# Kernel optimization log

Measured on AMD Instinct MI355X. Metric: run time of the kernel, lower is better.

## Reference

```python
import jax, jax.numpy as jnp
import numpy as np

EMBED = 768
HEADS = 12
HEAD_DIM = EMBED // HEADS
SCALE = HEAD_DIM ** -0.5


def setup_inputs() -> dict:
    key = jax.random.key(0)
    k1, k2, k3, k4, k5 = jax.random.split(key, 5)
    x = jax.random.normal(k1, (4, 2048, EMBED), dtype=jnp.float32)
    w_qkv = jax.random.normal(k2, (EMBED, 3 * EMBED), dtype=jnp.float32) * (EMBED ** -0.5)
    b_qkv = jax.random.normal(k3, (3 * EMBED,), dtype=jnp.float32) * 0.02
    w_proj = jax.random.normal(k4, (EMBED, EMBED), dtype=jnp.float32) * (EMBED ** -0.5)
    b_proj = jax.random.normal(k5, (EMBED,), dtype=jnp.float32) * 0.02
    return {"x": x, "w_qkv": w_qkv, "b_qkv": b_qkv, "w_proj": w_proj, "b_proj": b_proj}


def reference(x, w_qkv, b_qkv, w_proj, b_proj):
    B, T, D = x.shape
    qkv = x @ w_qkv + b_qkv                      # [B, T, 3D]
    qkv = qkv.reshape(B, T, 3, HEADS, HEAD_DIM)
    qkv = jnp.transpose(qkv, (2, 0, 3, 1, 4))    # [3, B, H, T, hd]
    q, k, v = qkv[0], qkv[1], qkv[2]
    scores = jnp.einsum('bhqd,bhkd->bhqk', q, k) * SCALE
    attn = jax.nn.softmax(scores, axis=-1)       # dropout p=0.0 -> identity
    out = jnp.einsum('bhqk,bhkd->bhqd', attn, v)
    out = jnp.transpose(out, (0, 2, 1, 3)).reshape(B, T, D)
    return out @ w_proj + b_proj
```

## Files before the change

### kernel.cpp

```cpp
#include <hip/hip_runtime.h>
#include <hip/hip_bf16.h>

#define EMBED 768
#define HEADS 12
#define HD 64
#define BATCH 4
#define SEQ 2048
#define M_TOK (BATCH*SEQ)
#define N_QKV (3*EMBED)
#define SL2E 0.18033688011112042f

typedef short bf8 __attribute__((ext_vector_type(8)));
typedef float f4  __attribute__((ext_vector_type(4)));
typedef unsigned short us8 __attribute__((ext_vector_type(8)));

static __device__ inline unsigned short f2bf(float f) {
    unsigned int x = __float_as_uint(f);
    unsigned int r = (x + 0x7fffu + ((x >> 16) & 1u)) >> 16;
    return (unsigned short)r;
}

static __device__ inline unsigned int pack2bf(float a, float b) {
#if defined(__has_builtin)
#if __has_builtin(__builtin_amdgcn_cvt_pk_bf16_f32)
    auto r = __builtin_amdgcn_cvt_pk_bf16_f32(a, b);
    return __builtin_bit_cast(unsigned int, r);
#else
    unsigned int ua = (__float_as_uint(a) + 0x8000u) >> 16;
    unsigned int ub = (__float_as_uint(b) + 0x8000u) & 0xffff0000u;
    return ua | ub;
#endif
#else
    unsigned int ua = (__float_as_uint(a) + 0x8000u) >> 16;
    unsigned int ub = (__float_as_uint(b) + 0x8000u) & 0xffff0000u;
    return ua | ub;
#endif
}

#define GLD_LDS(gp, lp) __builtin_amdgcn_global_load_lds( \
    (const __attribute__((address_space(1))) void*)(gp),  \
    (__attribute__((address_space(3))) void*)(lp), 16, 0, 0)

__global__ void cvt_f32_bf16(const float* __restrict__ in,
                             unsigned short* __restrict__ out, int n) {
    int i = (blockIdx.x * blockDim.x + threadIdx.x) * 4;
    if (i < n) {
        float4 v = *reinterpret_cast<const float4*>(in + i);
        ushort4 o;
        o.x = f2bf(v.x); o.y = f2bf(v.y); o.z = f2bf(v.z); o.w = f2bf(v.w);
        *reinterpret_cast<ushort4*>(out + i) = o;
    }
}

__global__ void transpose_f32_bf16(const float* __restrict__ in,
                                   unsigned short* __restrict__ out, int R, int C,
                                   float scale, int nlim) {
    __shared__ float tile[32][33];
    int c0 = blockIdx.x * 32, r0 = blockIdx.y * 32;
    int tx = threadIdx.x, ty = threadIdx.y;
    for (int i = 0; i < 32; i += 8)
        tile[ty + i][tx] = in[(size_t)(r0 + ty + i) * C + c0 + tx];
    __syncthreads();
    for (int i = 0; i < 32; i += 8) {
        int orow = c0 + ty + i;
        float s = (orow < nlim) ? scale : 1.0f;
        out[(size_t)orow * R + r0 + tx] = f2bf(tile[tx][ty + i] * s);
    }
}

__global__ void scale_bias(const float* __restrict__ in, float* __restrict__ out) {
    int i = blockIdx.x * 256 + threadIdx.x;
    if (i < N_QKV) out[i] = in[i] * (i < 768 ? SL2E : 1.0f);
}

template<int OUT_MODE>
__global__ __launch_bounds__(256) void gemm_bf16(
    const unsigned short* __restrict__ A,
    const unsigned short* __restrict__ BT,
    const float* __restrict__ bias,
    void* __restrict__ Cout, int M, int N, int K)
{
    const int LDA = 32;
    __shared__ unsigned short a_lds[128 * 32];
    __shared__ unsigned short b_lds[128 * 32];
    int tid  = threadIdx.x;
    int lane = tid & 63, w = tid >> 6;
    int quad = lane >> 4, cc = lane & 15;
    int m0 = blockIdx.x * 128, n0 = blockIdx.y * 128;
    int wr = w >> 1, wc = w & 1;
    int mb = wr * 64, nb = wc * 64;
    const unsigned short* Ab = A + (size_t)m0 * K;
    const unsigned short* Bb = BT + (size_t)n0 * K;
    f4 acc[4][4] = {};
    for (int k0 = 0; k0 < K; k0 += 32) {
        __syncthreads();
        for (int p = 0; p < 2; ++p) {
            int li  = p * 256 + tid;
            int row = li >> 2, ch = li & 3;
            GLD_LDS(Ab + (size_t)row * K + k0 + ch * 8, &a_lds[li * 8]);
            GLD_LDS(Bb + (size_t)row * K + k0 + ch * 8, &b_lds[li * 8]);
        }
        __syncthreads();
        bf8 af[4], bfv[4];
        for (int mi = 0; mi < 4; ++mi)
            af[mi] = *reinterpret_cast<const bf8*>(&a_lds[(mb + mi * 16 + cc) * LDA + quad * 8]);
        for (int ni = 0; ni < 4; ++ni)
            bfv[ni] = *reinterpret_cast<const bf8*>(&b_lds[(nb + ni * 16 + cc) * LDA + quad * 8]);
        for (int mi = 0; mi < 4; ++mi)
            for (int ni = 0; ni < 4; ++ni)
                acc[mi][ni] = __builtin_amdgcn_mfma_f32_16x16x32_bf16(af[mi], bfv[ni], acc[mi][ni], 0, 0, 0);
    }
    for (int mi = 0; mi < 4; ++mi)
        for (int ni = 0; ni < 4; ++ni) {
            int gn = n0 + nb + ni * 16 + cc;
            float bv = bias[gn];
            for (int r = 0; r < 4; ++r) {
                int gm = m0 + mb + mi * 16 + quad * 4 + r;
                float v = acc[mi][ni][r] + bv;
                if (OUT_MODE == 0)
                    ((unsigned short*)Cout)[(size_t)gm * N + gn] = f2bf(v);
                else
                    ((float*)Cout)[(size_t)gm * N + gn] = v;
            }
        }
}

__global__ __launch_bounds__(256) void vtrans(
    const unsigned short* __restrict__ qkv, unsigned short* __restrict__ vt)
{
    __shared__ unsigned short lds[64 * 72];
    int tid = threadIdx.x;
    int t0 = blockIdx.x * 64, h = blockIdx.y, b = blockIdx.z;
    for (int p = 0; p < 2; ++p) {
        int li = p * 256 + tid, row = li >> 3, col = li & 7;
        *reinterpret_cast<uint4*>(&lds[row * 72 + col * 8]) =
            *reinterpret_cast<const uint4*>(
                qkv + (size_t)(b * SEQ + t0 + row) * 2304 + 1536 + h * 64 + col * 8);
    }
    __syncthreads();
    for (int p = 0; p < 2; ++p) {
        int li = p * 256 + tid, d = li >> 3, tc = li & 7;
        us8 v;
        for (int j = 0; j < 8; ++j) v[j] = lds[(tc * 8 + j) * 72 + d];
        *reinterpret_cast<us8*>(
            vt + ((size_t)(b * HEADS + h) * 64 + d) * SEQ + t0 + tc * 8) = v;
    }
}

__global__ __launch_bounds__(512, 6) void attn_kernel(
    const unsigned short* __restrict__ qkv,
    const unsigned short* __restrict__ vt,
    unsigned short* __restrict__ out)
{
    const int LDK = 72;
    __shared__ unsigned short k_lds[64 * 72];
    __shared__ unsigned short v_lds[64 * 72];
    __shared__ unsigned short p_lds[128 * 72];
    int tid  = threadIdx.x;
    int lane = tid & 63, w = tid >> 6;
    int quad = lane >> 4, cc = lane & 15;
    int id  = blockIdx.x;
    int sub = id >> 3, rem = id & 7;
    int g   = (sub >> 4) * 8 + rem;
    int qt  = sub & 15;
    int b   = g / HEADS, h = g % HEADS;
    int q0  = qt * 128;

    bf8 qf[2];
    {
        const unsigned short* qp =
            qkv + (size_t)(b * SEQ + q0 + w * 16 + cc) * 2304 + h * 64;
        qf[0] = *reinterpret_cast<const bf8*>(qp + quad * 8);
        qf[1] = *reinterpret_cast<const bf8*>(qp + 32 + quad * 8);
    }
    f4 acc[4] = {};
    float lsum = 0.f;
    const unsigned short* kbase = qkv + (size_t)b * SEQ * 2304 + 768 + h * 64;
    const unsigned short* vbase = vt + (size_t)(b * HEADS + h) * 64 * SEQ;

    int srow = tid >> 3, scol = tid & 7;
    const unsigned short* kp = kbase + (size_t)srow * 2304 + scol * 8;
    const unsigned short* vp = vbase + (size_t)srow * SEQ + scol * 8;
    unsigned short* kl = &k_lds[srow * LDK + scol * 8];
    unsigned short* vl = &v_lds[srow * LDK + scol * 8];

    uint4 kr = *reinterpret_cast<const uint4*>(kp);
    uint4 vr = *reinterpret_cast<const uint4*>(vp);

    for (int kt = 0; kt < SEQ; kt += 64) {
        __syncthreads();
        *reinterpret_cast<uint4*>(kl) = kr;
        *reinterpret_cast<uint4*>(vl) = vr;
        __syncthreads();
        int ktn = kt + 64;
        if (ktn < SEQ) {
            kr = *reinterpret_cast<const uint4*>(kp + (size_t)ktn * 2304);
            vr = *reinterpret_cast<const uint4*>(vp + ktn);
        }
        for (int mt = 0; mt < 4; ++mt) {
            bf8 a0 = *reinterpret_cast<const bf8*>(&k_lds[(mt * 16 + cc) * LDK + quad * 8]);
            bf8 a1 = *reinterpret_cast<const bf8*>(&k_lds[(mt * 16 + cc) * LDK + 32 + quad * 8]);
            f4 z = {};
            z = __builtin_amdgcn_mfma_f32_16x16x32_bf16(a0, qf[0], z, 0, 0, 0);
            z = __builtin_amdgcn_mfma_f32_16x16x32_bf16(a1, qf[1], z, 0, 0, 0);
            float p0 = exp2f(z[0]), p1 = exp2f(z[1]), p2 = exp2f(z[2]), p3 = exp2f(z[3]);
            lsum += (p0 + p1) + (p2 + p3);
            uint2 pk;
            pk.x = pack2bf(p0, p1);
            pk.y = pack2bf(p2, p3);
            int ql = w * 16 + cc;
            *reinterpret_cast<uint2*>(&p_lds[ql * LDK + mt * 16 + quad * 4]) = pk;
        }
        bf8 a0 = *reinterpret_cast<const bf8*>(&p_lds[(w * 16 + cc) * LDK + quad * 8]);
        bf8 a1 = *reinterpret_cast<const bf8*>(&p_lds[(w * 16 + cc) * LDK + 32 + quad * 8]);
        for (int nt = 0; nt < 4; ++nt) {
            bf8 vb0 = *reinterpret_cast<const bf8*>(&v_lds[(nt * 16 + cc) * LDK + quad * 8]);
            bf8 vb1 = *reinterpret_cast<const bf8*>(&v_lds[(nt * 16 + cc) * LDK + 32 + quad * 8]);
            acc[nt] = __builtin_amdgcn_mfma_f32_16x16x32_bf16(a0, vb0, acc[nt], 0, 0, 0);
            acc[nt] = __builtin_amdgcn_mfma_f32_16x16x32_bf16(a1, vb1, acc[nt], 0, 0, 0);
        }
    }
    lsum += __shfl_xor(lsum, 16);
    lsum += __shfl_xor(lsum, 32);
    for (int r = 0; r < 4; ++r) {
        float L = __shfl(lsum, quad * 4 + r);
        float inv = 1.0f / L;
        int q = q0 + w * 16 + quad * 4 + r;
        size_t ob = (size_t)(b * SEQ + q) * 768 + h * 64;
        for (int nt = 0; nt < 4; ++nt)
            out[ob + nt * 16 + cc] = f2bf(acc[nt][r] * inv);
    }
}

extern "C" void kernel_launch(void* const* d_in, const int* in_sizes, int n_in,
                              void* d_out, int out_size, void* d_ws, size_t ws_size,
                              hipStream_t stream) {
    const float* x      = (const float*)d_in[0];
    const float* w_qkv  = (const float*)d_in[1];
    const float* b_qkv  = (const float*)d_in[2];
    const float* w_proj = (const float*)d_in[3];
    const float* b_proj = (const float*)d_in[4];
    float* out = (float*)d_out;
    char* ws = (char*)d_ws;
    unsigned short* qkv    = (unsigned short*)(ws);
    unsigned short* vt_buf = (unsigned short*)(ws + 37748736);
    unsigned short* aout   = (unsigned short*)(ws + 50331648);
    unsigned short* xbf    = aout;
    unsigned short* wqkvT  = (unsigned short*)(ws + 62914560);
    unsigned short* wprojT = (unsigned short*)(ws + 66453504);
    float*          bqkv_s = (float*)(ws + 67633152);

    cvt_f32_bf16<<<(M_TOK * EMBED) / 1024, 256, 0, stream>>>(x, xbf, M_TOK * EMBED);
    transpose_f32_bf16<<<dim3(N_QKV / 32, EMBED / 32), dim3(32, 8), 0, stream>>>(
        w_qkv, wqkvT, EMBED, N_QKV, SL2E, 768);
    transpose_f32_bf16<<<dim3(EMBED / 32, EMBED / 32), dim3(32, 8), 0, stream>>>(
        w_proj, wprojT, EMBED, EMBED, 1.0f, 0);
    scale_bias<<<9, 256, 0, stream>>>(b_qkv, bqkv_s);
    gemm_bf16<0><<<dim3(M_TOK / 128, N_QKV / 128), 256, 0, stream>>>(
        xbf, wqkvT, bqkv_s, qkv, M_TOK, N_QKV, EMBED);
    vtrans<<<dim3(SEQ / 64, HEADS, BATCH), 256, 0, stream>>>(qkv, vt_buf);
    attn_kernel<<<768, 512, 0, stream>>>(qkv, vt_buf, aout);
    gemm_bf16<1><<<dim3(M_TOK / 128, EMBED / 128), 256, 0, stream>>>(
        aout, wprojT, b_proj, out, M_TOK, EMBED, EMBED);
}
```

Measured before the change: 250.8 us.

## Switch attention to 32x32x16 MFMA tiles with split-K across wave pairs

New measurement: 304.6 us. 1.21x slower.

```diff
diff --git a/kernel.cpp b/kernel.cpp
--- a/kernel.cpp
+++ b/kernel.cpp
@@ -12,6 +12,7 @@
 
 typedef short bf8 __attribute__((ext_vector_type(8)));
 typedef float f4  __attribute__((ext_vector_type(4)));
+typedef float f16v __attribute__((ext_vector_type(16)));
 typedef unsigned short us8 __attribute__((ext_vector_type(8)));
 
 static __device__ inline unsigned short f2bf(float f) {
@@ -153,12 +154,14 @@
     unsigned short* __restrict__ out)
 {
     const int LDK = 72;
-    __shared__ unsigned short k_lds[64 * 72];
-    __shared__ unsigned short v_lds[64 * 72];
-    __shared__ unsigned short p_lds[128 * 72];
+    __shared__ unsigned short smem[18432];
+    unsigned short* k_lds = smem;
+    unsigned short* v_lds = smem + 4608;
+    unsigned short* p_lds = smem + 9216;
     int tid  = threadIdx.x;
     int lane = tid & 63, w = tid >> 6;
-    int quad = lane >> 4, cc = lane & 15;
+    int ln   = lane & 31, hk = lane >> 5;
+    int qq   = w >> 1, kh = w & 1;
     int id  = blockIdx.x;
     int sub = id >> 3, rem = id & 7;
     int g   = (sub >> 4) * 8 + rem;
@@ -166,14 +169,16 @@
     int b   = g / HEADS, h = g % HEADS;
     int q0  = qt * 128;
 
-    bf8 qf[2];
+    bf8 qf[4];
     {
         const unsigned short* qp =
-            qkv + (size_t)(b * SEQ + q0 + w * 16 + cc) * 2304 + h * 64;
-        qf[0] = *reinterpret_cast<const bf8*>(qp + quad * 8);
-        qf[1] = *reinterpret_cast<const bf8*>(qp + 32 + quad * 8);
-    }
-    f4 acc[4] = {};
+            qkv + (size_t)(b * SEQ + q0 + qq * 32 + ln) * 2304 + h * 64 + hk * 8;
+        qf[0] = *reinterpret_cast<const bf8*>(qp);
+        qf[1] = *reinterpret_cast<const bf8*>(qp + 16);
+        qf[2] = *reinterpret_cast<const bf8*>(qp + 32);
+        qf[3] = *reinterpret_cast<const bf8*>(qp + 48);
+    }
+    f16v acc[2] = {};
     float lsum = 0.f;
     const unsigned short* kbase = qkv + (size_t)b * SEQ * 2304 + 768 + h * 64;
     const unsigned short* vbase = vt + (size_t)(b * HEADS + h) * 64 * SEQ;
@@ -186,6 +191,9 @@
 
     uint4 kr = *reinterpret_cast<const uint4*>(kp);
     uint4 vr = *reinterpret_cast<const uint4*>(vp);
+
+    int prow  = (qq * 32 + ln) * LDK + kh * 32 + hk * 4;
+    int parow = (qq * 32 + ln) * LDK + kh * 32 + hk * 8;
 
     for (int kt = 0; kt < SEQ; kt += 64) {
         __syncthreads();
@@ -197,38 +205,70 @@
             kr = *reinterpret_cast<const uint4*>(kp + (size_t)ktn * 2304);
             vr = *reinterpret_cast<const uint4*>(vp + ktn);
         }
-        for (int mt = 0; mt < 4; ++mt) {
-            bf8 a0 = *reinterpret_cast<const bf8*>(&k_lds[(mt * 16 + cc) * LDK + quad * 8]);
-            bf8 a1 = *reinterpret_cast<const bf8*>(&k_lds[(mt * 16 + cc) * LDK + 32 + quad * 8]);
-            f4 z = {};
-            z = __builtin_amdgcn_mfma_f32_16x16x32_bf16(a0, qf[0], z, 0, 0, 0);
-            z = __builtin_amdgcn_mfma_f32_16x16x32_bf16(a1, qf[1], z, 0, 0, 0);
-            float p0 = exp2f(z[0]), p1 = exp2f(z[1]), p2 = exp2f(z[2]), p3 = exp2f(z[3]);
+        f16v z = {};
+        {
+            int krow = (kh * 32 + ln) * LDK + hk * 8;
+            bf8 a0 = *reinterpret_cast<const bf8*>(&k_lds[krow]);
+            bf8 a1 = *reinterpret_cast<const bf8*>(&k_lds[krow + 16]);
+            bf8 a2 = *reinterpret_cast<const bf8*>(&k_lds[krow + 32]);
+            bf8 a3 = *reinterpret_cast<const bf8*>(&k_lds[krow + 48]);
+            z = __builtin_amdgcn_mfma_f32_32x32x16_bf16(a0, qf[0], z, 0, 0, 0);
+            z = __builtin_amdgcn_mfma_f32_32x32x16_bf16(a1, qf[1], z, 0, 0, 0);
+            z = __builtin_amdgcn_mfma_f32_32x32x16_bf16(a2, qf[2], z, 0, 0, 0);
+            z = __builtin_amdgcn_mfma_f32_32x32x16_bf16(a3, qf[3], z, 0, 0, 0);
+        }
+        for (int gg = 0; gg < 4; ++gg) {
+            float p0 = exp2f(z[4 * gg]),     p1 = exp2f(z[4 * gg + 1]);
+            float p2 = exp2f(z[4 * gg + 2]), p3 = exp2f(z[4 * gg + 3]);
             lsum += (p0 + p1) + (p2 + p3);
             uint2 pk;
             pk.x = pack2bf(p0, p1);
             pk.y = pack2bf(p2, p3);
-            int ql = w * 16 + cc;
-            *reinterpret_cast<uint2*>(&p_lds[ql * LDK + mt * 16 + quad * 4]) = pk;
-        }
-        bf8 a0 = *reinterpret_cast<const bf8*>(&p_lds[(w * 16 + cc) * LDK + quad * 8]);
-        bf8 a1 = *reinterpret_cast<const bf8*>(&p_lds[(w * 16 + cc) * LDK + 32 + quad * 8]);
-        for (int nt = 0; nt < 4; ++nt) {
-            bf8 vb0 = *reinterpret_cast<const bf8*>(&v_lds[(nt * 16 + cc) * LDK + quad * 8]);
-            bf8 vb1 = *reinterpret_cast<const bf8*>(&v_lds[(nt * 16 + cc) * LDK + 32 + quad * 8]);
-            acc[nt] = __builtin_amdgcn_mfma_f32_16x16x32_bf16(a0, vb0, acc[nt], 0, 0, 0);
-            acc[nt] = __builtin_amdgcn_mfma_f32_16x16x32_bf16(a1, vb1, acc[nt], 0, 0, 0);
-        }
-    }
-    lsum += __shfl_xor(lsum, 16);
+            *reinterpret_cast<uint2*>(&p_lds[prow + gg * 8]) = pk;
+        }
+        bf8 pa0 = *reinterpret_cast<const bf8*>(&p_lds[parow]);
+        bf8 pa1 = *reinterpret_cast<const bf8*>(&p_lds[parow + 16]);
+        for (int db = 0; db < 2; ++db) {
+            int vrow = (db * 32 + ln) * LDK + kh * 32 + hk * 8;
+            bf8 v0 = *reinterpret_cast<const bf8*>(&v_lds[vrow]);
+            bf8 v1 = *reinterpret_cast<const bf8*>(&v_lds[vrow + 16]);
+            acc[db] = __builtin_amdgcn_mfma_f32_32x32x16_bf16(pa0, v0, acc[db], 0, 0, 0);
+            acc[db] = __builtin_amdgcn_mfma_f32_32x32x16_bf16(pa1, v1, acc[db], 0, 0, 0);
+        }
+    }
     lsum += __shfl_xor(lsum, 32);
-    for (int r = 0; r < 4; ++r) {
-        float L = __shfl(lsum, quad * 4 + r);
-        float inv = 1.0f / L;
-        int q = q0 + w * 16 + quad * 4 + r;
-        size_t ob = (size_t)(b * SEQ + q) * 768 + h * 64;
-        for (int nt = 0; nt < 4; ++nt)
-            out[ob + nt * 16 + cc] = f2bf(acc[nt][r] * inv);
+    __syncthreads();
+    float* olds  = reinterpret_cast<float*>(smem);
+    float* l_lds = olds + 8192;
+    if (kh) {
+        for (int db = 0; db < 2; ++db)
+            for (int gg = 0; gg < 4; ++gg) {
+                float4 vv = { acc[db][4 * gg], acc[db][4 * gg + 1],
+                              acc[db][4 * gg + 2], acc[db][4 * gg + 3] };
+                *reinterpret_cast<float4*>(&olds[(qq * 2 + db) * 1024 + gg * 256 + lane * 4]) = vv;
+            }
+        if (lane < 32) l_lds[qq * 32 + lane] = lsum;
+    }
+    __syncthreads();
+    if (!kh) {
+        float linv = 1.0f / (lsum + l_lds[qq * 32 + ln]);
+        for (int db = 0; db < 2; ++db)
+            for (int gg = 0; gg < 4; ++gg) {
+                float4 vv = *reinterpret_cast<float4*>(
+                    &olds[(qq * 2 + db) * 1024 + gg * 256 + lane * 4]);
+                acc[db][4 * gg]     += vv.x;
+                acc[db][4 * gg + 1] += vv.y;
+                acc[db][4 * gg + 2] += vv.z;
+                acc[db][4 * gg + 3] += vv.w;
+            }
+        for (int db = 0; db < 2; ++db)
+            for (int reg = 0; reg < 16; ++reg) {
+                int qrow = (reg & 3) + 8 * (reg >> 2) + 4 * hk;
+                float li = __shfl(linv, qrow);
+                int q = q0 + qq * 32 + qrow;
+                out[(size_t)(b * SEQ + q) * 768 + h * 64 + db * 32 + ln] =
+                    f2bf(acc[db][reg] * li);
+            }
     }
 }
 
```
